# Optimization experiments

Hardware: AMD Instinct MI355X
Metric: run time of the kernel (lower is better)

Reference implementation:

```python
import jax, jax.numpy as jnp
import numpy as np

BN_EPS = 1e-5

def _bn_relu(x, gamma, beta):
    # x: [B, C, N]; BatchNorm1d in training mode: stats over (B, N) per channel
    mean = jnp.mean(x, axis=(0, 2), keepdims=True)
    var = jnp.var(x, axis=(0, 2), keepdims=True)
    xn = (x - mean) * jax.lax.rsqrt(var + BN_EPS)
    return jax.nn.relu(xn * gamma[None, :, None] + beta[None, :, None])


def setup_inputs() -> dict:
    key = jax.random.key(0)
    ks = jax.random.split(key, 8)
    B, N, S, D1, D2 = 16, 4096, 1024, 64, 256
    C_in, H = D1 + D2, 256  # mlp_list = [320, 256, 256]
    inp = {
        "xyz1": jax.random.normal(ks[0], (B, 3, N), jnp.float32),
        "xyz2": jax.random.normal(ks[1], (B, 3, S), jnp.float32),
        "points1": jax.random.normal(ks[2], (B, D1, N), jnp.float32),
        "points2": jax.random.normal(ks[3], (B, D2, S), jnp.float32),
        # 1x1 Conv1d weights of the SeqLinear pointNet MLP
        "W1": jax.random.normal(ks[4], (H, C_in), jnp.float32) / np.sqrt(C_in),
        "b1": jnp.zeros((H,), jnp.float32),
        "g1": jnp.ones((H,), jnp.float32),
        "bt1": jnp.zeros((H,), jnp.float32),
        "W2": jax.random.normal(ks[5], (H, H), jnp.float32) / np.sqrt(H),
        "b2": jnp.zeros((H,), jnp.float32),
        "g2": jnp.ones((H,), jnp.float32),
        "bt2": jnp.zeros((H,), jnp.float32),
    }
    return inp


def reference(xyz1, xyz2, points1, points2, W1, b1, g1, bt1, W2, b2, g2, bt2):
    x1 = jnp.transpose(xyz1, (0, 2, 1))   # [B, N, 3]
    x2 = jnp.transpose(xyz2, (0, 2, 1))   # [B, S, 3]
    p2 = jnp.transpose(points2, (0, 2, 1))  # [B, S, D2]
    B, N, _ = x1.shape

    # square_distance: ||x1||^2 + ||x2||^2 - 2 x1.x2  -> [B, N, S]
    dists = (jnp.sum(x1 * x1, axis=-1, keepdims=True)
             + jnp.sum(x2 * x2, axis=-1)[:, None, :]
             - 2.0 * jnp.einsum('bnc,bsc->bns', x1, x2))

    # 3 nearest neighbors (smallest distances)
    neg_d3, idx = jax.lax.top_k(-dists, 3)   # [B, N, 3]
    d3 = -neg_d3
    recip = 1.0 / (d3 + 1e-8)
    weight = recip / jnp.sum(recip, axis=2, keepdims=True)  # [B, N, 3]

    # gather neighbor features: [B, N, 3, D2]
    gathered = jax.vmap(lambda p, i: p[i])(p2, idx)
    interp = jnp.sum(gathered * weight[..., None], axis=2)  # [B, N, D2]

    new_points = jnp.concatenate([jnp.transpose(points1, (0, 2, 1)), interp], axis=-1)
    x = jnp.transpose(new_points, (0, 2, 1))  # [B, 320, N]

    # pointNet MLP: conv1x1 -> BN -> ReLU, twice
    h = jnp.einsum('oc,bcn->bon', W1, x) + b1[None, :, None]
    h = _bn_relu(h, g1, bt1)
    h = jnp.einsum('oc,bcn->bon', W2, h) + b2[None, :, None]
    h = _bn_relu(h, g2, bt2)
    return h
```

## Files before the change

kernel.cpp:

```cpp
#include <hip/hip_runtime.h>
#include <cstddef>

#define B_   16
#define N_   4096
#define S_   1024
#define D1_  64
#define D2_  256
#define CIN_ 320
#define H_   256
#define CH_  8
#define SC_  (S_ / CH_)
#define P_   (B_ * (N_ / 128))

using short8 = __attribute__((ext_vector_type(8))) short;
using f32x4  = __attribute__((ext_vector_type(4))) float;

typedef const __attribute__((address_space(1))) unsigned g1u32;
typedef __attribute__((address_space(3))) unsigned l3u32;

__device__ __forceinline__ void gl_lds16(const void* g, void* l) {
  __builtin_amdgcn_global_load_lds((g1u32*)g, (l3u32*)l, 16, 0, 0);
}

__device__ __forceinline__ float relu_f(float v) { return fmaxf(v, 0.0f); }

__device__ __forceinline__ ushort f2bf(float f) {
  unsigned u = __builtin_bit_cast(unsigned, f);
  u += 0x7fffu + ((u >> 16) & 1u);
  return (ushort)(u >> 16);
}
__device__ __forceinline__ float bf2f(ushort u) {
  return __builtin_bit_cast(float, (unsigned)u << 16);
}

__global__ __launch_bounds__(256) void prep_knn(
    const float* __restrict__ points2, const float* __restrict__ W1,
    const float* __restrict__ W2, const float* __restrict__ xyz1,
    const float* __restrict__ xyz2, ushort* __restrict__ p2tb,
    ushort* __restrict__ W1b, ushort* __restrict__ W2b,
    float* __restrict__ pd, int* __restrict__ pi) {
  __shared__ union { float tile[32][33]; float4 P[SC_]; } sm;
  int g = blockIdx.x, t = threadIdx.x;
  if (g < 4096) {
    int z = g >> 8, rem = g & 255;
    int c0 = (rem & 31) * 32;
    int r0 = (rem >> 5) * 32;
    const float* in = points2 + (size_t)z * D2_ * S_;
    ushort* out = p2tb + (size_t)z * S_ * D2_;
    int tx = t & 31, ty = t >> 5;
#pragma unroll
    for (int j = 0; j < 4; ++j) {
      int r = r0 + ty + j * 8;
      sm.tile[ty + j * 8][tx] = in[(size_t)r * S_ + c0 + tx];
    }
    __syncthreads();
#pragma unroll
    for (int j = 0; j < 4; ++j) {
      int c = c0 + ty + j * 8;
      out[(size_t)c * D2_ + r0 + tx] = f2bf(sm.tile[tx][ty + j * 8]);
    }
  } else if (g < 4168) {
    int g2 = g - 4096;
    const float* src = (g2 < 40) ? W1 : W2;
    ushort* dst = (g2 < 40) ? W1b : W2b;
    int base = ((g2 < 40) ? g2 : g2 - 40) * 2048 + t * 8;
    float4 a = *(const float4*)&src[base];
    float4 b = *(const float4*)&src[base + 4];
    short8 r;
    r[0] = (short)f2bf(a.x); r[1] = (short)f2bf(a.y);
    r[2] = (short)f2bf(a.z); r[3] = (short)f2bf(a.w);
    r[4] = (short)f2bf(b.x); r[5] = (short)f2bf(b.y);
    r[6] = (short)f2bf(b.z); r[7] = (short)f2bf(b.w);
    *(short8*)&dst[base] = r;
  } else {
    int gk = g - 4168;
    int b = gk & 15;
    int ch = (gk >> 4) & 7;
    int n = (gk >> 7) * 256 + t;
    const float* x2b = xyz2 + (size_t)b * 3 * S_ + ch * SC_;
    if (t < SC_) {
      float x = x2b[t], y = x2b[S_ + t], z = x2b[2 * S_ + t];
      sm.P[t] = make_float4(-2.f * x, -2.f * y, -2.f * z, x * x + y * y + z * z);
    }
    __syncthreads();

    const float* x1b = xyz1 + (size_t)b * 3 * N_;
    float px = x1b[n], py = x1b[N_ + n], pz = x1b[2 * N_ + n];
    float sq1 = px * px + py * py + pz * pz;

    float d0 = 1e30f, d1 = 1e30f, d2 = 1e30f;
    int i0 = 0, i1 = 0, i2 = 0;
#pragma unroll 4
    for (int s = 0; s < SC_; ++s) {
      float4 p = sm.P[s];
      float d = fmaf(px, p.x, fmaf(py, p.y, fmaf(pz, p.z, p.w)));
      int gi = ch * SC_ + s;
      if (d < d2) {
        if (d < d1) {
          if (d < d0) { d2 = d1; i2 = i1; d1 = d0; i1 = i0; d0 = d; i0 = gi; }
          else        { d2 = d1; i2 = i1; d1 = d;  i1 = gi; }
        } else        { d2 = d;  i2 = gi; }
      }
    }
    size_t base = (((size_t)b * N_ + n) * CH_ + ch) * 3;
    pd[base] = d0 + sq1; pd[base + 1] = d1 + sq1; pd[base + 2] = d2 + sq1;
    pi[base] = i0; pi[base + 1] = i1; pi[base + 2] = i2;
  }
}

__global__ __launch_bounds__(256) void build_fused(
    const float* __restrict__ points1,
    const ushort* __restrict__ p2tb,
    const float* __restrict__ pd, const int* __restrict__ pi,
    ushort* __restrict__ xt) {
  __shared__ int   lidx[16][3];
  __shared__ float lw[16][3];
  __shared__ ushort p1t[16][72];
  int g = blockIdx.x, t = threadIdx.x;
  int b = g & 15;
  int p0 = (g >> 4) * 16;

  if (t < 16) {
    size_t pb = (size_t)b * N_ + p0 + t;
    const float* pdp = pd + pb * 24;
    const int*   pip = pi + pb * 24;
    float d0 = 1e30f, d1 = 1e30f, d2 = 1e30f;
    int i0 = 0, i1 = 0, i2 = 0;
#pragma unroll
    for (int k = 0; k < 24; ++k) {
      float d = pdp[k];
      int gi = pip[k];
      if (d < d2) {
        if (d < d1) {
          if (d < d0) { d2 = d1; i2 = i1; d1 = d0; i1 = i0; d0 = d; i0 = gi; }
          else        { d2 = d1; i2 = i1; d1 = d;  i1 = gi; }
        } else        { d2 = d;  i2 = gi; }
      }
    }
    float r0 = 1.0f / (d0 + 1e-8f);
    float r1 = 1.0f / (d1 + 1e-8f);
    float r2 = 1.0f / (d2 + 1e-8f);
    float rs = 1.0f / (r0 + r1 + r2);
    lidx[t][0] = i0; lidx[t][1] = i1; lidx[t][2] = i2;
    lw[t][0] = r0 * rs; lw[t][1] = r1 * rs; lw[t][2] = r2 * rs;
  }

  {
    int c = t >> 2, q4 = t & 3;
    float4 v = *(const float4*)&points1[((size_t)b * D1_ + c) * N_ + p0 + q4 * 4];
    p1t[q4 * 4 + 0][c] = f2bf(v.x);
    p1t[q4 * 4 + 1][c] = f2bf(v.y);
    p1t[q4 * 4 + 2][c] = f2bf(v.z);
    p1t[q4 * 4 + 3][c] = f2bf(v.w);
  }
  __syncthreads();

  int pl = t >> 4, q = t & 15;
  size_t pb = (size_t)b * N_ + p0 + pl;
  int i0 = lidx[pl][0], i1 = lidx[pl][1], i2 = lidx[pl][2];
  float w0 = lw[pl][0], w1 = lw[pl][1], w2 = lw[pl][2];
  const ushort* R0 = p2tb + ((size_t)b * S_ + i0) * D2_;
  const ushort* R1 = p2tb + ((size_t)b * S_ + i1) * D2_;
  const ushort* R2 = p2tb + ((size_t)b * S_ + i2) * D2_;
  ushort* o = xt + pb * CIN_;

  if (q < 8)
    *(short8*)(o + q * 8) = *(const short8*)&p1t[pl][q * 8];

#pragma unroll
  for (int it = 0; it < 2; ++it) {
    int c = it * 16 + q;
    short8 a = *(const short8*)&R0[c * 8];
    short8 d = *(const short8*)&R1[c * 8];
    short8 e = *(const short8*)&R2[c * 8];
    short8 r;
#pragma unroll
    for (int u = 0; u < 8; ++u) {
      float v = w0 * bf2f((ushort)a[u]) + w1 * bf2f((ushort)d[u]) +
                w2 * bf2f((ushort)e[u]);
      r[u] = (short)f2bf(v);
    }
    *(short8*)(o + D1_ + c * 8) = r;
  }
}

template <int K, bool BNIN>
__global__ __launch_bounds__(256) void gemm_pipe(
    const ushort* __restrict__ Wb, const ushort* __restrict__ Xt,
    const float* __restrict__ bias, const float* __restrict__ scin,
    const float* __restrict__ shin, ushort* __restrict__ Yt,
    float* __restrict__ ps1, float* __restrict__ ps2) {
  constexpr int NT = K / 64;
  __shared__ union SM {
    struct { ushort A[2][128][64]; ushort Bt[2][128][64]; } st;
    struct { ushort C[128][132]; float S1[128][33]; float S2[128][33]; } ep;
  } sm;
  __shared__ float scs_l[H_], shs_l[H_];

  int b  = blockIdx.z;
  int n0 = blockIdx.x * 128;
  int m0 = blockIdx.y * 128;
  int tid = threadIdx.x;
  int lane = tid & 63, wid = tid >> 6;
  int wm = (wid >> 1) * 64, wn = (wid & 1) * 64;
  int lr = lane & 15, hi = lane >> 4;
  size_t bn0 = (size_t)b * N_ + n0;

  if (BNIN) {
    for (int i = tid; i < K; i += 256) { scs_l[i] = scin[i]; shs_l[i] = shin[i]; }
  }

  const char* Agb = (const char*)(Wb + (size_t)m0 * K);
  const char* Bgb = (const char*)(Xt + bn0 * K);
  const size_t rowB = (size_t)K * 2;

  size_t gsrc[4];
  int    ldst[4];
#pragma unroll
  for (int r = 0; r < 4; ++r) {
    int m = (wid * 4 + r) * 64 + lane;
    int row = m >> 3;
    int c = ((m & 7) - row) & 7;
    gsrc[r] = (size_t)row * rowB + (size_t)c * 16;
    ldst[r] = m * 16;
  }

  auto stage = [&](int buf, int kc) {
    char* bA = (char*)sm.st.A[buf];
    char* bB = (char*)sm.st.Bt[buf];
    size_t kb = (size_t)kc * 128;
#pragma unroll
    for (int r = 0; r < 4; ++r) {
      gl_lds16(Agb + gsrc[r] + kb, bA + ldst[r]);
      gl_lds16(Bgb + gsrc[r] + kb, bB + ldst[r]);
    }
  };

  f32x4 acc[4][4] = {};

  stage(0, 0);
  __syncthreads();

  int cur = 0;
  for (int t = 0; t < NT; ++t) {
    if (t + 1 < NT) stage(cur ^ 1, t + 1);
#pragma unroll
    for (int ks = 0; ks < 2; ++ks) {
      short8 af[4], bv[4];
#pragma unroll
      for (int i = 0; i < 4; ++i) {
        int rA = wm + i * 16 + lr;
        int rB = wn + i * 16 + lr;
        int sA = (rA + ks * 4 + hi) & 7;
        int sB = (rB + ks * 4 + hi) & 7;
        af[i] = *(const short8*)&sm.st.A[cur][rA][sA * 8];
        bv[i] = *(const short8*)&sm.st.Bt[cur][rB][sB * 8];
      }
      if (BNIN) {
        int kb = t * 64 + ks * 32 + hi * 8;
        f32x4 sa = *(const f32x4*)&scs_l[kb];
        f32x4 sb = *(const f32x4*)&scs_l[kb + 4];
        f32x4 ha = *(const f32x4*)&shs_l[kb];
        f32x4 hb = *(const f32x4*)&shs_l[kb + 4];
#pragma unroll
        for (int i = 0; i < 4; ++i) {
          short8 pk;
#pragma unroll
          for (int e = 0; e < 4; ++e) {
            pk[e]     = (short)f2bf(relu_f(bf2f((ushort)bv[i][e]) * sa[e] + ha[e]));
            pk[e + 4] = (short)f2bf(relu_f(bf2f((ushort)bv[i][e + 4]) * sb[e] + hb[e]));
          }
          bv[i] = pk;
        }
      }
#pragma unroll
      for (int mf = 0; mf < 4; ++mf)
#pragma unroll
        for (int nf = 0; nf < 4; ++nf)
          acc[mf][nf] = __builtin_amdgcn_mfma_f32_16x16x32_bf16(
              af[mf], bv[nf], acc[mf][nf], 0, 0, 0);
    }
    __syncthreads();
    cur ^= 1;
  }

  float sum1[4][4] = {}, sum2[4][4] = {};
#pragma unroll
  for (int mf = 0; mf < 4; ++mf) {
#pragma unroll
    for (int nf = 0; nf < 4; ++nf) {
      int n = wn + nf * 16 + lr;
      ushort4 u;
#pragma unroll
      for (int j = 0; j < 4; ++j) {
        float v = acc[mf][nf][j] + bias[m0 + wm + mf * 16 + hi * 4 + j];
        sum1[mf][j] += v;
        sum2[mf][j] += v * v;
        ((ushort*)&u)[j] = f2bf(v);
      }
      *(ushort4*)&sm.ep.C[n][wm + mf * 16 + hi * 4] = u;
    }
  }
  __syncthreads();
  {
    int rown = tid >> 4, q = tid & 15;
#pragma unroll
    for (int p = 0; p < 8; ++p) {
      int n = p * 16 + rown;
      short8 val = *(const short8*)&sm.ep.C[n][q * 8];
      *(short8*)&Yt[(bn0 + n) * H_ + m0 + q * 8] = val;
    }
  }
  int col = (wid & 1) * 16 + lr;
#pragma unroll
  for (int mf = 0; mf < 4; ++mf)
#pragma unroll
    for (int j = 0; j < 4; ++j) {
      int c = wm + mf * 16 + hi * 4 + j;
      sm.ep.S1[c][col] = sum1[mf][j];
      sm.ep.S2[c][col] = sum2[mf][j];
    }
  __syncthreads();
  int pidx = b * gridDim.x + blockIdx.x;
  int c = tid & 127;
  float s = 0.f;
  if (tid < 128) {
#pragma unroll
    for (int k = 0; k < 32; ++k) s += sm.ep.S1[c][k];
    ps1[(size_t)pidx * H_ + m0 + c] = s;
  } else {
#pragma unroll
    for (int k = 0; k < 32; ++k) s += sm.ep.S2[c][k];
    ps2[(size_t)pidx * H_ + m0 + c] = s;
  }
}

__global__ __launch_bounds__(256) void bn_stats_fin(
    const float* __restrict__ ps1, const float* __restrict__ ps2,
    const float* __restrict__ gamma, const float* __restrict__ beta,
    float* __restrict__ sc, float* __restrict__ sh) {
  int c = blockIdx.x, t = threadIdx.x;
  float s1 = ps1[(size_t)t * H_ + c] + ps1[(size_t)(t + 256) * H_ + c];
  float s2 = ps2[(size_t)t * H_ + c] + ps2[(size_t)(t + 256) * H_ + c];
  __shared__ float S1[256], S2[256];
  S1[t] = s1; S2[t] = s2;
  __syncthreads();
  for (int off = 128; off > 0; off >>= 1) {
    if (t < off) { S1[t] += S1[t + off]; S2[t] += S2[t + off]; }
    __syncthreads();
  }
  if (t == 0) {
    const float inv = 1.0f / (float)(B_ * N_);
    float mean = S1[0] * inv;
    float var  = S2[0] * inv - mean * mean;
    float g    = gamma[c] * rsqrtf(var + 1e-5f);
    sc[c] = g;
    sh[c] = beta[c] - mean * g;
  }
}

__global__ __launch_bounds__(256) void bn_out_t(
    const ushort* __restrict__ Hb, const float* __restrict__ sc,
    const float* __restrict__ sh, float* __restrict__ out) {
  __shared__ float tile[32][132];
  int b = blockIdx.z;
  int n0 = blockIdx.x * 32, m0 = blockIdx.y * 128;
  int t = threadIdx.x;
  int m8 = (t & 15) * 8;
  f32x4 sa = *(const f32x4*)&sc[m0 + m8];
  f32x4 sb = *(const f32x4*)&sc[m0 + m8 + 4];
  f32x4 ha = *(const f32x4*)&sh[m0 + m8];
  f32x4 hb = *(const f32x4*)&sh[m0 + m8 + 4];
  size_t bn0 = (size_t)b * N_ + n0;
#pragma unroll
  for (int pass = 0; pass < 2; ++pass) {
    int n = pass * 16 + (t >> 4);
    short8 v = *(const short8*)&Hb[(bn0 + n) * H_ + m0 + m8];
#pragma unroll
    for (int e = 0; e < 4; ++e) {
      tile[n][m8 + e]     = relu_f(bf2f((ushort)v[e]) * sa[e] + ha[e]);
      tile[n][m8 + 4 + e] = relu_f(bf2f((ushort)v[e + 4]) * sb[e] + hb[e]);
    }
  }
  __syncthreads();
  int m = t >> 1, nh = (t & 1) * 16;
  float* orow = out + ((size_t)b * H_ + m0 + m) * N_ + n0 + nh;
#pragma unroll
  for (int j = 0; j < 4; ++j) {
    float4 v;
    v.x = tile[nh + j * 4 + 0][m];
    v.y = tile[nh + j * 4 + 1][m];
    v.z = tile[nh + j * 4 + 2][m];
    v.w = tile[nh + j * 4 + 3][m];
    *(float4*)&orow[j * 4] = v;
  }
}

extern "C" void kernel_launch(void* const* d_in, const int* in_sizes, int n_in,
                              void* d_out, int out_size, void* d_ws,
                              size_t ws_size, hipStream_t stream) {
  const float* xyz1    = (const float*)d_in[0];
  const float* xyz2    = (const float*)d_in[1];
  const float* points1 = (const float*)d_in[2];
  const float* points2 = (const float*)d_in[3];
  const float* W1  = (const float*)d_in[4];
  const float* b1  = (const float*)d_in[5];
  const float* g1  = (const float*)d_in[6];
  const float* bt1 = (const float*)d_in[7];
  const float* W2  = (const float*)d_in[8];
  const float* b2  = (const float*)d_in[9];
  const float* g2  = (const float*)d_in[10];
  const float* bt2 = (const float*)d_in[11];
  float* out = (float*)d_out;
  char* cur = (char*)d_ws;
  auto alloc = [&](size_t bytes) { char* p = cur; cur += (bytes + 255) & ~255ull; return p; };

  ushort* p2tb = (ushort*)alloc((size_t)B_ * S_ * D2_ * 2);
  float*  pd   = (float*)alloc((size_t)B_ * N_ * CH_ * 3 * 4);
  int*    pi   = (int*)alloc((size_t)B_ * N_ * CH_ * 3 * 4);
  ushort* W1b  = (ushort*)alloc((size_t)H_ * CIN_ * 2);
  ushort* W2b  = (ushort*)alloc((size_t)H_ * H_ * 2);
  ushort* xct  = (ushort*)alloc((size_t)B_ * N_ * CIN_ * 2);
  ushort* h1t  = (ushort*)alloc((size_t)B_ * N_ * H_ * 2);
  float*  ps1  = (float*)alloc((size_t)P_ * H_ * 4);
  float*  ps2  = (float*)alloc((size_t)P_ * H_ * 4);
  float*  sc1  = (float*)alloc(H_ * 4);
  float*  sh1  = (float*)alloc(H_ * 4);
  float*  sc2  = (float*)alloc(H_ * 4);
  float*  sh2  = (float*)alloc(H_ * 4);
  ushort* h2b  = xct;

  prep_knn<<<4096 + 40 + 32 + 2048, 256, 0, stream>>>(
      points2, W1, W2, xyz1, xyz2, p2tb, W1b, W2b, pd, pi);

  build_fused<<<B_ * N_ / 16, 256, 0, stream>>>(points1, p2tb, pd, pi, xct);

  gemm_pipe<CIN_, false><<<dim3(N_ / 128, H_ / 128, B_), 256, 0, stream>>>(
      W1b, xct, b1, nullptr, nullptr, h1t, ps1, ps2);
  bn_stats_fin<<<H_, 256, 0, stream>>>(ps1, ps2, g1, bt1, sc1, sh1);

  gemm_pipe<H_, true><<<dim3(N_ / 128, H_ / 128, B_), 256, 0, stream>>>(
      W2b, h1t, b2, sc1, sh1, h2b, ps1, ps2);
  bn_stats_fin<<<H_, 256, 0, stream>>>(ps1, ps2, g2, bt2, sc2, sh2);

  bn_out_t<<<dim3(N_ / 32, H_ / 128, B_), 256, 0, stream>>>(h2b, sc2, sh2, out);
}
```

Before: 156.6 us.

## Apply BN-ReLU once at B-tile staging and use packed bf16 conversion

In the second GEMM the input BN+ReLU was previously recomputed on every fragment read by every warp. Now each B tile is loaded into registers, normalised once, and written to LDS, with the global load issued before the MFMA loop and the LDS write after it, so the load overlaps compute. Separately, the scalar float-to-bf16 rounding sequences are replaced with the hardware packed v_cvt_pk_bf16_f32 instruction throughout. The trade-off is losing direct global-to-LDS DMA for that GEMM's B operand and paying extra register pressure for the staged values.

```diff
diff --git a/kernel.cpp b/kernel.cpp
--- a/kernel.cpp
+++ b/kernel.cpp
@@ -28,6 +28,11 @@
   unsigned u = __builtin_bit_cast(unsigned, f);
   u += 0x7fffu + ((u >> 16) & 1u);
   return (ushort)(u >> 16);
+}
+__device__ __forceinline__ unsigned f2bf2(float a, float b) {
+  unsigned r;
+  asm("v_cvt_pk_bf16_f32 %0, %1, %2" : "=v"(r) : "v"(a), "v"(b));
+  return r;
 }
 __device__ __forceinline__ float bf2f(ushort u) {
   return __builtin_bit_cast(float, (unsigned)u << 16);
@@ -67,10 +72,10 @@
     float4 a = *(const float4*)&src[base];
     float4 b = *(const float4*)&src[base + 4];
     short8 r;
-    r[0] = (short)f2bf(a.x); r[1] = (short)f2bf(a.y);
-    r[2] = (short)f2bf(a.z); r[3] = (short)f2bf(a.w);
-    r[4] = (short)f2bf(b.x); r[5] = (short)f2bf(b.y);
-    r[6] = (short)f2bf(b.z); r[7] = (short)f2bf(b.w);
+    ((unsigned*)&r)[0] = f2bf2(a.x, a.y);
+    ((unsigned*)&r)[1] = f2bf2(a.z, a.w);
+    ((unsigned*)&r)[2] = f2bf2(b.x, b.y);
+    ((unsigned*)&r)[3] = f2bf2(b.z, b.w);
     *(short8*)&dst[base] = r;
   } else {
     int gk = g - 4168;
@@ -175,10 +180,12 @@
     short8 e = *(const short8*)&R2[c * 8];
     short8 r;
 #pragma unroll
-    for (int u = 0; u < 8; ++u) {
-      float v = w0 * bf2f((ushort)a[u]) + w1 * bf2f((ushort)d[u]) +
-                w2 * bf2f((ushort)e[u]);
-      r[u] = (short)f2bf(v);
+    for (int u = 0; u < 4; ++u) {
+      float v0 = w0 * bf2f((ushort)a[2 * u]) + w1 * bf2f((ushort)d[2 * u]) +
+                 w2 * bf2f((ushort)e[2 * u]);
+      float v1 = w0 * bf2f((ushort)a[2 * u + 1]) + w1 * bf2f((ushort)d[2 * u + 1]) +
+                 w2 * bf2f((ushort)e[2 * u + 1]);
+      ((unsigned*)&r)[u] = f2bf2(v0, v1);
     }
     *(short8*)(o + D1_ + c * 8) = r;
   }
@@ -211,11 +218,13 @@
   }
 
   const char* Agb = (const char*)(Wb + (size_t)m0 * K);
-  const char* Bgb = (const char*)(Xt + bn0 * K);
+  const ushort* Bg = Xt + bn0 * K;
+  const char* Bgb = (const char*)Bg;
   const size_t rowB = (size_t)K * 2;
 
   size_t gsrc[4];
   int    ldst[4];
+  int    brow[4], bcol[4];
 #pragma unroll
   for (int r = 0; r < 4; ++r) {
     int m = (wid * 4 + r) * 64 + lane;
@@ -223,27 +232,65 @@
     int c = ((m & 7) - row) & 7;
     gsrc[r] = (size_t)row * rowB + (size_t)c * 16;
     ldst[r] = m * 16;
-  }
-
-  auto stage = [&](int buf, int kc) {
+    brow[r] = row; bcol[r] = c;
+  }
+
+  auto stageA = [&](int buf, int kc) {
     char* bA = (char*)sm.st.A[buf];
+    size_t kb = (size_t)kc * 128;
+#pragma unroll
+    for (int r = 0; r < 4; ++r)
+      gl_lds16(Agb + gsrc[r] + kb, bA + ldst[r]);
+  };
+  auto stageB_dma = [&](int buf, int kc) {
     char* bB = (char*)sm.st.Bt[buf];
     size_t kb = (size_t)kc * 128;
 #pragma unroll
+    for (int r = 0; r < 4; ++r)
+      gl_lds16(Bgb + gsrc[r] + kb, bB + ldst[r]);
+  };
+
+  short8 braw[4];
+  auto loadB = [&](int kc) {
+#pragma unroll
+    for (int r = 0; r < 4; ++r)
+      braw[r] = *(const short8*)&Bg[(size_t)brow[r] * K + kc * 64 + bcol[r] * 8];
+  };
+  auto writeB = [&](int buf, int kc) {
+#pragma unroll
     for (int r = 0; r < 4; ++r) {
-      gl_lds16(Agb + gsrc[r] + kb, bA + ldst[r]);
-      gl_lds16(Bgb + gsrc[r] + kb, bB + ldst[r]);
+      int kb = kc * 64 + bcol[r] * 8;
+      short8 pk;
+#pragma unroll
+      for (int u = 0; u < 4; ++u) {
+        float y0 = relu_f(bf2f((ushort)braw[r][2 * u]) * scs_l[kb + 2 * u] +
+                          shs_l[kb + 2 * u]);
+        float y1 = relu_f(bf2f((ushort)braw[r][2 * u + 1]) * scs_l[kb + 2 * u + 1] +
+                          shs_l[kb + 2 * u + 1]);
+        ((unsigned*)&pk)[u] = f2bf2(y0, y1);
+      }
+      *(short8*)((char*)sm.st.Bt[buf] + ldst[r]) = pk;
     }
   };
 
   f32x4 acc[4][4] = {};
 
-  stage(0, 0);
+  stageA(0, 0);
+  if (BNIN) {
+    loadB(0);
+    __syncthreads();
+    writeB(0, 0);
+  } else {
+    stageB_dma(0, 0);
+  }
   __syncthreads();
 
   int cur = 0;
   for (int t = 0; t < NT; ++t) {
-    if (t + 1 < NT) stage(cur ^ 1, t + 1);
+    if (t + 1 < NT) {
+      stageA(cur ^ 1, t + 1);
+      if (BNIN) loadB(t + 1); else stageB_dma(cur ^ 1, t + 1);
+    }
 #pragma unroll
     for (int ks = 0; ks < 2; ++ks) {
       short8 af[4], bv[4];
@@ -256,23 +303,6 @@
         af[i] = *(const short8*)&sm.st.A[cur][rA][sA * 8];
         bv[i] = *(const short8*)&sm.st.Bt[cur][rB][sB * 8];
       }
-      if (BNIN) {
-        int kb = t * 64 + ks * 32 + hi * 8;
-        f32x4 sa = *(const f32x4*)&scs_l[kb];
-        f32x4 sb = *(const f32x4*)&scs_l[kb + 4];
-        f32x4 ha = *(const f32x4*)&shs_l[kb];
-        f32x4 hb = *(const f32x4*)&shs_l[kb + 4];
-#pragma unroll
-        for (int i = 0; i < 4; ++i) {
-          short8 pk;
-#pragma unroll
-          for (int e = 0; e < 4; ++e) {
-            pk[e]     = (short)f2bf(relu_f(bf2f((ushort)bv[i][e]) * sa[e] + ha[e]));
-            pk[e + 4] = (short)f2bf(relu_f(bf2f((ushort)bv[i][e + 4]) * sb[e] + hb[e]));
-          }
-          bv[i] = pk;
-        }
-      }
 #pragma unroll
       for (int mf = 0; mf < 4; ++mf)
 #pragma unroll
@@ -280,6 +310,7 @@
           acc[mf][nf] = __builtin_amdgcn_mfma_f32_16x16x32_bf16(
               af[mf], bv[nf], acc[mf][nf], 0, 0, 0);
     }
+    if (BNIN && t + 1 < NT) writeB(cur ^ 1, t + 1);
     __syncthreads();
     cur ^= 1;
   }
@@ -290,14 +321,16 @@
 #pragma unroll
     for (int nf = 0; nf < 4; ++nf) {
       int n = wn + nf * 16 + lr;
+      float v[4];
+#pragma unroll
+      for (int j = 0; j < 4; ++j) {
+        v[j] = acc[mf][nf][j] + bias[m0 + wm + mf * 16 + hi * 4 + j];
+        sum1[mf][j] += v[j];
+        sum2[mf][j] += v[j] * v[j];
+      }
       ushort4 u;
-#pragma unroll
-      for (int j = 0; j < 4; ++j) {
-        float v = acc[mf][nf][j] + bias[m0 + wm + mf * 16 + hi * 4 + j];
-        sum1[mf][j] += v;
-        sum2[mf][j] += v * v;
-        ((ushort*)&u)[j] = f2bf(v);
-      }
+      ((unsigned*)&u)[0] = f2bf2(v[0], v[1]);
+      ((unsigned*)&u)[1] = f2bf2(v[2], v[3]);
       *(ushort4*)&sm.ep.C[n][wm + mf * 16 + hi * 4] = u;
     }
   }
```

After: 154.7 us. About the same (-1.2%).
